# Kernel optimization log

Hardware: AMD Instinct MI355X
Metric: run time of the kernel (lower is better)

## Reference

```python
import jax, jax.numpy as jnp
import numpy as np

GAMMA = 2.0
EPS = 1e-12  # tf.nn.l2_normalize epsilon


def setup_inputs() -> dict:
    key = jax.random.key(0)
    k1, k2 = jax.random.split(key)
    B, H, W_, C = 8, 56, 56, 256
    x = jax.random.normal(k1, (B, H, W_, C), dtype=jnp.float32)
    W = jax.random.normal(k2, (C, C), dtype=jnp.float32) * 0.05
    return {"x": x, "W": W}


def reference(x, W):
    B, H, Wd, C = x.shape
    hw = H * Wd
    # transform branch: 1x1 conv, no bias (num_layers=1)
    t = jnp.einsum('bhwc,cd->bhwd', x, W).reshape(B, hw, C)
    # pixel affinity: cosine similarity (tf: -cosine_similarity == cos sim)
    xf = x.reshape(B, hw, C)
    inv_norm = jax.lax.rsqrt(jnp.maximum(jnp.sum(xf * xf, axis=-1, keepdims=True), EPS))
    xn = xf * inv_norm
    sim = jnp.einsum('bic,bjc->bij', xn, xn)  # [B, hw, hw]
    sim = jnp.power(jax.nn.relu(sim), GAMMA)
    y = jnp.einsum('bij,bjc->bic', sim, t)
    return y.reshape(B, H, Wd, C)
```

## Files before the change

### kernel.cpp

```cpp
#include <hip/hip_runtime.h>

#define HW 3136
#define CH 256
#define NJT 49
#define NIT 25
#define NPIX 25088

typedef __attribute__((ext_vector_type(8))) short bf16x8;
typedef __attribute__((ext_vector_type(4))) float f32x4;
typedef __attribute__((ext_vector_type(16))) float f32x16;
typedef unsigned short u16;
typedef unsigned int u32;

static __device__ __forceinline__ u16 f2bf(float f){
  union { float f; u32 u; } v; v.f = f;
  u32 r = v.u + 0x7FFFu + ((v.u >> 16) & 1u);
  return (u16)(r >> 16);
}

static __device__ __forceinline__ void gload16(const void* g, void* l){
  __builtin_amdgcn_global_load_lds(
      (const __attribute__((address_space(1))) unsigned int*)g,
      (__attribute__((address_space(3))) unsigned int*)l, 16, 0, 0);
}

static __device__ __forceinline__ f32x16 zero16(){
  f32x16 v;
  #pragma unroll
  for (int e = 0; e < 16; ++e) v[e] = 0.f;
  return v;
}

#define MFMA32(A,B,C) __builtin_amdgcn_mfma_f32_32x32x16_bf16((A),(B),(C),0,0,0)

__global__ __launch_bounds__(256) void prep_wt(const float* __restrict__ W,
                                               u16* __restrict__ Wt){
  const int o = blockIdx.x, i = threadIdx.x;
  Wt[o*CH + i] = f2bf(W[i*CH + o]);
}

__global__ __launch_bounds__(256) void gemm_t(const float* __restrict__ x,
                                              const u16* __restrict__ Wt,
                                              u16* __restrict__ xn_bf,
                                              u16* __restrict__ tT){
  __shared__ u16 sT[256*64];
  const int jt = blockIdx.x, b = blockIdx.y;
  const int tid = threadIdx.x, wid = tid >> 6, lane = tid & 63;
  const int l15 = lane & 15, l4 = lane >> 4;
  const int j0 = jt * 64;
  const int row = j0 + wid*16 + l15;
  const float* xp = x + ((size_t)b*HW + row)*CH + l4*8;

  float xv[8][8];
  float ss = 0.f;
  #pragma unroll
  for (int kb = 0; kb < 8; ++kb){
    const float4 v0 = *(const float4*)(xp + kb*32);
    const float4 v1 = *(const float4*)(xp + kb*32 + 4);
    xv[kb][0]=v0.x; xv[kb][1]=v0.y; xv[kb][2]=v0.z; xv[kb][3]=v0.w;
    xv[kb][4]=v1.x; xv[kb][5]=v1.y; xv[kb][6]=v1.z; xv[kb][7]=v1.w;
    #pragma unroll
    for (int e = 0; e < 8; ++e) ss += xv[kb][e]*xv[kb][e];
  }
  ss += __shfl_xor(ss, 16);
  ss += __shfl_xor(ss, 32);
  const float inv = rsqrtf(fmaxf(ss, 1e-12f));

  bf16x8 ax[8];
  #pragma unroll
  for (int kb = 0; kb < 8; ++kb){
    bf16x8 a, n;
    #pragma unroll
    for (int e = 0; e < 8; ++e){
      a[e] = (short)f2bf(xv[kb][e]);
      n[e] = (short)f2bf(xv[kb][e]*inv);
    }
    ax[kb] = a;
    *(bf16x8*)(xn_bf + ((size_t)b*HW + row)*CH + kb*32 + l4*8) = n;
  }

  f32x4 acc[16];
  #pragma unroll
  for (int n = 0; n < 16; ++n) acc[n] = f32x4{0.f,0.f,0.f,0.f};
  #pragma unroll
  for (int kb = 0; kb < 8; ++kb){
    #pragma unroll
    for (int n0 = 0; n0 < 16; ++n0){
      const bf16x8 bb = *(const bf16x8*)(Wt + (n0*16 + l15)*CH + kb*32 + l4*8);
      acc[n0] = __builtin_amdgcn_mfma_f32_16x16x32_bf16(ax[kb], bb, acc[n0], 0, 0, 0);
    }
  }
  #pragma unroll
  for (int n0 = 0; n0 < 16; ++n0){
    const int c = n0*16 + l15;
    const int jloc = wid*16 + l4*4;
    const int gj = jloc >> 3;
    ushort4 w4;
    w4.x = f2bf(acc[n0][0]); w4.y = f2bf(acc[n0][1]);
    w4.z = f2bf(acc[n0][2]); w4.w = f2bf(acc[n0][3]);
    *(ushort4*)&sT[c*64 + ((gj ^ (c & 7)) * 8) + (jloc & 7)] = w4;
  }
  __syncthreads();
  #pragma unroll
  for (int p = 0; p < 8; ++p){
    const int c = p*32 + (tid >> 3);
    const int q = tid & 7;
    const bf16x8 v = *(const bf16x8*)&sT[c*64 + ((q ^ (c & 7)) * 8)];
    *(bf16x8*)(tT + ((size_t)b*CH + c)*HW + j0 + q*8) = v;
  }
}

__global__ __launch_bounds__(512) void ppm_main(const u16* __restrict__ xn,
                                                const u16* __restrict__ tT,
                                                float* __restrict__ out){
  __shared__ u16 SM[81920];

  const int bid = blockIdx.x;
  const int swz = (bid & 7)*25 + (bid >> 3);
  const int b = swz / 25;
  const int it = swz % 25;

  const int tid = threadIdx.x, wid = tid >> 6, lane = tid & 63;
  const int l31 = lane & 31, hi = lane >> 5;
  const int i0 = it * 128;
  const int wj = wid >> 2, wi = wid & 3;
  const int ih = wi >> 1, cq = wj*2 + (wi & 1);

  bf16x8 aq[16];
  {
    int irow = i0 + wi*32 + l31;
    if (irow >= HW) irow = HW - 1;
    const u16* p = xn + ((size_t)b*HW + irow)*CH + hi*8;
    #pragma unroll
    for (int ks = 0; ks < 16; ++ks) aq[ks] = *(const bf16x8*)(p + ks*16);
  }

  f32x16 accY[2][2];
  #pragma unroll
  for (int cb = 0; cb < 2; ++cb)
    #pragma unroll
    for (int ibx = 0; ibx < 2; ++ibx) accY[cb][ibx] = zero16();

  const size_t xbase = (size_t)b*HW;
  const size_t tbase = (size_t)b*CH;

  auto STAGE_XN = [&](int jt){
    u16* dst = SM + (jt & 1)*16384;
    const int j0n = jt*64;
    #pragma unroll
    for (int q = 0; q < 4; ++q){
      const int m = q*512 + tid;
      const int row = m >> 5, g = m & 31;
      gload16(xn + (xbase + j0n + row)*CH + ((g ^ (row & 15))*8), &dst[m*8]);
    }
  };
  auto STAGE_TT = [&](int jt){
    u16* dst = SM + 32768 + (jt & 1)*16384;
    const int j0n = jt*64;
    #pragma unroll
    for (int q = 0; q < 4; ++q){
      const int m = q*512 + tid;
      const int c = m >> 3, g = m & 7;
      gload16(tT + (tbase + c)*HW + j0n + ((g ^ (c & 7))*8), &dst[m*8]);
    }
  };

  auto PV = [&](int p){
    const u16* sTJp = SM + 32768 + (p & 1)*16384;
    const u16* sPBp = SM + 65536 + (p & 1)*8192;
    bf16x8 pb[4][2];
    #pragma unroll
    for (int ks = 0; ks < 4; ++ks)
      #pragma unroll
      for (int ibx = 0; ibx < 2; ++ibx)
        pb[ks][ibx] = *(const bf16x8*)&sPBp[((ih*2 + ibx)*4 + ks)*512 + lane*8];
    __builtin_amdgcn_s_setprio(1);
    #pragma unroll
    for (int ks = 0; ks < 4; ++ks){
      #pragma unroll
      for (int cb = 0; cb < 2; ++cb){
        const int c = cq*64 + cb*32 + l31;
        const bf16x8 af = *(const bf16x8*)&sTJp[c*64 + (((ks*2 + hi) ^ (c & 7)) * 8)];
        #pragma unroll
        for (int ibx = 0; ibx < 2; ++ibx)
          accY[cb][ibx] = MFMA32(af, pb[ks][ibx], accY[cb][ibx]);
      }
    }
    __builtin_amdgcn_s_setprio(0);
  };

  STAGE_XN(0);
  __syncthreads();

  #pragma unroll 1
  for (int jt = 0; jt < NJT; ++jt){
    if (jt + 1 < NJT) STAGE_XN(jt + 1);
    STAGE_TT(jt);

    if (jt > 0) PV(jt - 1);

    const u16* sXJk = SM + (jt & 1)*16384;
    f32x16 sa = zero16(), sb = zero16();
    const int rj = wj*32 + l31;
    const int rsw = rj & 15;
    const u16* xjrow = &sXJk[rj*256];
    __builtin_amdgcn_s_setprio(1);
    #pragma unroll
    for (int kb = 0; kb < 8; ++kb){
      const bf16x8 a0 = *(const bf16x8*)&xjrow[(((kb*4 + hi)     ^ rsw) * 8)];
      const bf16x8 a1 = *(const bf16x8*)&xjrow[(((kb*4 + 2 + hi) ^ rsw) * 8)];
      sa = MFMA32(a0, aq[2*kb],   sa);
      sb = MFMA32(a1, aq[2*kb+1], sb);
    }
    __builtin_amdgcn_s_setprio(0);

    float s0,s1,s2,s3,s4,s5,s6,s7,s8,s9,s10,s11,s12,s13,s14,s15;
#define SREL(d, r) { float v_ = sa[r] + sb[r]; v_ = fmaxf(v_, 0.f); d = v_ * v_; }
    SREL(s0,0) SREL(s1,1) SREL(s2,2) SREL(s3,3) SREL(s4,4) SREL(s5,5) SREL(s6,6) SREL(s7,7)
    SREL(s8,8) SREL(s9,9) SREL(s10,10) SREL(s11,11) SREL(s12,12) SREL(s13,13) SREL(s14,14) SREL(s15,15)
#undef SREL
    u32 w0,w1,w2,w3,w4,w5,w6,w7;
#define PK(d, a, c) asm("v_cvt_pk_bf16_f32 %0, %1, %2" : "=v"(d) : "v"(a), "v"(c));
    PK(w0, s0, s1)  PK(w1, s2, s3)  PK(w2, s4, s5)  PK(w3, s6, s7)
    PK(w4, s8, s9)  PK(w5, s10,s11) PK(w6, s12,s13) PK(w7, s14,s15)
#undef PK
    asm volatile("v_permlane32_swap_b32 %0, %1" : "+v"(w0), "+v"(w2));
    asm volatile("v_permlane32_swap_b32 %0, %1" : "+v"(w1), "+v"(w3));
    asm volatile("v_permlane32_swap_b32 %0, %1" : "+v"(w4), "+v"(w6));
    asm volatile("v_permlane32_swap_b32 %0, %1" : "+v"(w5), "+v"(w7));
    union { u32 u[4]; bf16x8 v; } fb0, fb1;
    fb0.u[0]=w0; fb0.u[1]=w1; fb0.u[2]=w2; fb0.u[3]=w3;
    fb1.u[0]=w4; fb1.u[1]=w5; fb1.u[2]=w6; fb1.u[3]=w7;

    u16* sPBk = SM + 65536 + (jt & 1)*8192;
    *(bf16x8*)&sPBk[(wi*4 + 2*wj + 0)*512 + lane*8] = fb0.v;
    *(bf16x8*)&sPBk[(wi*4 + 2*wj + 1)*512 + lane*8] = fb1.v;

    __syncthreads();
  }

  PV(NJT - 1);
  __syncthreads();

  float* Yl = (float*)SM;
  {
    #pragma unroll
    for (int cb = 0; cb < 2; ++cb)
      #pragma unroll
      for (int ibx = 0; ibx < 2; ++ibx){
        const int il = ih*64 + ibx*32 + l31;
        const int isw = (il & 7) << 2;
        #pragma unroll
        for (int r = 0; r < 16; ++r){
          const int c = cq*64 + cb*32 + (r & 3) + 8*(r >> 2) + 4*hi;
          Yl[il*256 + (c ^ isw)] = accY[cb][ibx][r];
        }
      }
  }
  __syncthreads();
  {
    const int i3 = tid >> 2;
    const int cq4 = (tid & 3) * 64;
    const int sw3 = (i3 & 7) << 2;
    if (i0 + i3 < HW){
      float* orow = out + ((size_t)b*HW + i0 + i3)*CH;
      #pragma unroll
      for (int q = 0; q < 16; ++q){
        const int c = cq4 + q*4;
        const float4 v = *(const float4*)&Yl[i3*256 + (c ^ sw3)];
        *(float4*)&orow[c] = v;
      }
    }
  }
}

extern "C" void kernel_launch(void* const* d_in, const int* in_sizes, int n_in,
                              void* d_out, int out_size, void* d_ws, size_t ws_size,
                              hipStream_t stream){
  const float* x = (const float*)d_in[0];
  const float* W = (const float*)d_in[1];
  float* out = (float*)d_out;
  char* ws = (char*)d_ws;

  const size_t SZ = (size_t)NPIX * CH * sizeof(u16);
  u16* xn_bf = (u16*)(ws);
  u16* tT    = (u16*)(ws + SZ);
  u16* Wt    = (u16*)(ws + 2*SZ);

  prep_wt<<<CH, CH, 0, stream>>>(W, Wt);
  gemm_t<<<dim3(NJT, 8), 256, 0, stream>>>(x, Wt, xn_bf, tT);
  ppm_main<<<200, 512, 0, stream>>>(xn_bf, tT, out);
}
```

Before: 153.1 us.

## Load transform tile directly from global into registers instead of staging through LDS

Drops the LDS double-buffer for the transposed transform tile. Each wave now reads its own MFMA A-operand fragments straight from global memory into registers early in the iteration, then issues the PV MFMAs after the similarity tile is written. This shrinks shared memory per block and removes the LDS writes and reads for tT. In exchange each wave issues its own global loads with less coalescing, partly duplicated across waves, and global latency must be hidden by the QK compute.

```diff
diff --git a/kernel.cpp b/kernel.cpp
--- a/kernel.cpp
+++ b/kernel.cpp
@@ -113,7 +113,7 @@
 __global__ __launch_bounds__(512) void ppm_main(const u16* __restrict__ xn,
                                                 const u16* __restrict__ tT,
                                                 float* __restrict__ out){
-  __shared__ u16 SM[81920];
+  __shared__ u16 SM[65536];
 
   const int bid = blockIdx.x;
   const int swz = (bid & 7)*25 + (bid >> 3);
@@ -154,40 +154,6 @@
       gload16(xn + (xbase + j0n + row)*CH + ((g ^ (row & 15))*8), &dst[m*8]);
     }
   };
-  auto STAGE_TT = [&](int jt){
-    u16* dst = SM + 32768 + (jt & 1)*16384;
-    const int j0n = jt*64;
-    #pragma unroll
-    for (int q = 0; q < 4; ++q){
-      const int m = q*512 + tid;
-      const int c = m >> 3, g = m & 7;
-      gload16(tT + (tbase + c)*HW + j0n + ((g ^ (c & 7))*8), &dst[m*8]);
-    }
-  };
-
-  auto PV = [&](int p){
-    const u16* sTJp = SM + 32768 + (p & 1)*16384;
-    const u16* sPBp = SM + 65536 + (p & 1)*8192;
-    bf16x8 pb[4][2];
-    #pragma unroll
-    for (int ks = 0; ks < 4; ++ks)
-      #pragma unroll
-      for (int ibx = 0; ibx < 2; ++ibx)
-        pb[ks][ibx] = *(const bf16x8*)&sPBp[((ih*2 + ibx)*4 + ks)*512 + lane*8];
-    __builtin_amdgcn_s_setprio(1);
-    #pragma unroll
-    for (int ks = 0; ks < 4; ++ks){
-      #pragma unroll
-      for (int cb = 0; cb < 2; ++cb){
-        const int c = cq*64 + cb*32 + l31;
-        const bf16x8 af = *(const bf16x8*)&sTJp[c*64 + (((ks*2 + hi) ^ (c & 7)) * 8)];
-        #pragma unroll
-        for (int ibx = 0; ibx < 2; ++ibx)
-          accY[cb][ibx] = MFMA32(af, pb[ks][ibx], accY[cb][ibx]);
-      }
-    }
-    __builtin_amdgcn_s_setprio(0);
-  };
 
   STAGE_XN(0);
   __syncthreads();
@@ -195,9 +161,18 @@
   #pragma unroll 1
   for (int jt = 0; jt < NJT; ++jt){
     if (jt + 1 < NJT) STAGE_XN(jt + 1);
-    STAGE_TT(jt);
-
-    if (jt > 0) PV(jt - 1);
+
+    bf16x8 af[4][2];
+    if (jt > 0){
+      const int j0p = (jt - 1)*64;
+      #pragma unroll
+      for (int ks = 0; ks < 4; ++ks)
+        #pragma unroll
+        for (int cb = 0; cb < 2; ++cb){
+          const int c = cq*64 + cb*32 + l31;
+          af[ks][cb] = *(const bf16x8*)(tT + (tbase + c)*HW + j0p + ks*16 + hi*8);
+        }
+    }
 
     const u16* sXJk = SM + (jt & 1)*16384;
     f32x16 sa = zero16(), sb = zero16();
@@ -232,14 +207,57 @@
     fb0.u[0]=w0; fb0.u[1]=w1; fb0.u[2]=w2; fb0.u[3]=w3;
     fb1.u[0]=w4; fb1.u[1]=w5; fb1.u[2]=w6; fb1.u[3]=w7;
 
-    u16* sPBk = SM + 65536 + (jt & 1)*8192;
+    u16* sPBk = SM + 32768 + (jt & 1)*8192;
     *(bf16x8*)&sPBk[(wi*4 + 2*wj + 0)*512 + lane*8] = fb0.v;
     *(bf16x8*)&sPBk[(wi*4 + 2*wj + 1)*512 + lane*8] = fb1.v;
 
+    if (jt > 0){
+      const u16* sPBp = SM + 32768 + ((jt - 1) & 1)*8192;
+      bf16x8 pb[4][2];
+      #pragma unroll
+      for (int ks = 0; ks < 4; ++ks)
+        #pragma unroll
+        for (int ibx = 0; ibx < 2; ++ibx)
+          pb[ks][ibx] = *(const bf16x8*)&sPBp[((ih*2 + ibx)*4 + ks)*512 + lane*8];
+      __builtin_amdgcn_s_setprio(1);
+      #pragma unroll
+      for (int ks = 0; ks < 4; ++ks)
+        #pragma unroll
+        for (int cb = 0; cb < 2; ++cb)
+          #pragma unroll
+          for (int ibx = 0; ibx < 2; ++ibx)
+            accY[cb][ibx] = MFMA32(af[ks][cb], pb[ks][ibx], accY[cb][ibx]);
+      __builtin_amdgcn_s_setprio(0);
+    }
+
     __syncthreads();
   }
 
-  PV(NJT - 1);
+  {
+    const int j0p = (NJT - 1)*64;
+    bf16x8 af[4][2];
+    #pragma unroll
+    for (int ks = 0; ks < 4; ++ks)
+      #pragma unroll
+      for (int cb = 0; cb < 2; ++cb){
+        const int c = cq*64 + cb*32 + l31;
+        af[ks][cb] = *(const bf16x8*)(tT + (tbase + c)*HW + j0p + ks*16 + hi*8);
+      }
+    const u16* sPBp = SM + 32768 + ((NJT - 1) & 1)*8192;
+    bf16x8 pb[4][2];
+    #pragma unroll
+    for (int ks = 0; ks < 4; ++ks)
+      #pragma unroll
+      for (int ibx = 0; ibx < 2; ++ibx)
+        pb[ks][ibx] = *(const bf16x8*)&sPBp[((ih*2 + ibx)*4 + ks)*512 + lane*8];
+    #pragma unroll
+    for (int ks = 0; ks < 4; ++ks)
+      #pragma unroll
+      for (int cb = 0; cb < 2; ++cb)
+        #pragma unroll
+        for (int ibx = 0; ibx < 2; ++ibx)
+          accY[cb][ibx] = MFMA32(af[ks][cb], pb[ks][ibx], accY[cb][ibx]);
+  }
   __syncthreads();
 
   float* Yl = (float*)SM;
```

Result: slower. 186.5 us (+21.8%).
